# Optimization experiments

Hardware: AMD Instinct MI355X
Metric: run time of the kernel (lower is better)

## Reference

```python
import jax, jax.numpy as jnp
import numpy as np
from jax import lax

E = 8          # num_experts
K = 2          # top-k
TASKS = 8
GATE_DIM = 16
# (in, expand, out, kernel, stride) per MoE stage
STAGES = [(3, 32, 16, 7, 2), (16, 64, 32, 3, 1), (32, 128, 64, 3, 2), (64, 256, 64, 3, 1), (64, 128, 32, 3, 1)]
DN = ('NCHW', 'OIHW', 'NCHW')


def _pw(x, w):
    return lax.conv_general_dilated(x, w, (1, 1), 'VALID', dimension_numbers=DN)


def _dw(x, w, s):
    p = w.shape[-1] // 2
    return lax.conv_general_dilated(x, w, (s, s), [(p, p), (p, p)], dimension_numbers=DN, feature_group_count=x.shape[1])


def _gn(x, scale, bias):
    # GroupNorm with num_groups = C // 4, eps = 1e-5 (torch default)
    B, C, H, W = x.shape
    G = C // 4
    xr = x.reshape(B, G, -1)
    m = xr.mean(-1, keepdims=True)
    v = xr.var(-1, keepdims=True)
    xn = ((xr - m) * lax.rsqrt(v + 1e-5)).reshape(B, C, H, W)
    return xn * scale[None, :, None, None] + bias[None, :, None, None]


def _dsc(x, p, stride):
    # DSCBlock: pw-conv -> GN -> SiLU -> dw-conv -> GN -> SiLU -> pw-conv -> GN
    w1, s1, b1, w2, s2, b2, w3, s3, b3 = p
    x = jax.nn.silu(_gn(_pw(x, w1), s1, b1))
    x = jax.nn.silu(_gn(_dw(x, w2, stride), s2, b2))
    return _gn(_pw(x, w3), s3, b3)


def _moe(gate_input, x, wg, p, stride, task_bh):
    # task-conditioned top-k softmax gating (noisy_gating=False, all aux loss weights 0)
    logits = gate_input @ wg[task_bh]                      # (B, E)
    probs = jax.nn.softmax(logits, axis=-1)
    topv, topi = lax.top_k(probs, K)
    topv = topv / topv.sum(-1, keepdims=True)              # renormalize top-k gates
    Bn = gate_input.shape[0]
    dense = jnp.zeros_like(probs).at[jnp.arange(Bn)[:, None], topi].set(topv)
    eo = jax.vmap(lambda pe: _dsc(x, pe, stride))(p)       # (E, B, C, H, W)
    return jnp.einsum('be,ebchw->bchw', dense, eo)


def _forward(fl, task_bh):
    gi, xi, ppe = fl[0], fl[1], fl[2]
    x = xi
    for i, (_, _, _, _, s) in enumerate(STAGES):
        base = 3 + i * 10
        wg = fl[base]
        p = tuple(fl[base + 1: base + 10])
        x = _moe(gi, x, wg, p, s, task_bh)
    Bn = x.shape[0]
    # patchify: (B,32,20,20) -> unfold(2,4,4).unfold(3,4,4) -> permute -> (B,25,512)
    patches = x.reshape(Bn, 32, 5, 4, 5, 4).transpose(0, 1, 2, 4, 3, 5)  # (B,32,5,5,4,4)
    patches = patches.transpose(0, 2, 3, 4, 5, 1).reshape(Bn, 25, 512)
    return patches + ppe


def setup_inputs():
    key = jax.random.key(0)
    ks = iter(jax.random.split(key, 256))
    B = 64
    d = {}
    d['gate_input'] = jax.random.normal(next(ks), (B, GATE_DIM), jnp.float32)
    d['expert_input'] = jax.random.normal(next(ks), (B, 3, 80, 80), jnp.float32)
    d['patch_pos_embed'] = 0.02 * jax.random.normal(next(ks), (1, 25, 512), jnp.float32)
    for i, (cin, exp, cout, k, s) in enumerate(STAGES, 1):
        d[f's{i}_wg'] = 0.1 * jax.random.normal(next(ks), (TASKS, GATE_DIM, E), jnp.float32)
        d[f's{i}_w1'] = jax.random.normal(next(ks), (E, exp, cin, 1, 1), jnp.float32) / np.sqrt(cin)
        d[f's{i}_g1s'] = 1.0 + 0.1 * jax.random.normal(next(ks), (E, exp), jnp.float32)
        d[f's{i}_g1b'] = 0.1 * jax.random.normal(next(ks), (E, exp), jnp.float32)
        d[f's{i}_w2'] = jax.random.normal(next(ks), (E, exp, 1, k, k), jnp.float32) / k
        d[f's{i}_g2s'] = 1.0 + 0.1 * jax.random.normal(next(ks), (E, exp), jnp.float32)
        d[f's{i}_g2b'] = 0.1 * jax.random.normal(next(ks), (E, exp), jnp.float32)
        d[f's{i}_w3'] = jax.random.normal(next(ks), (E, cout, exp, 1, 1), jnp.float32) / np.sqrt(exp)
        d[f's{i}_g3s'] = 1.0 + 0.1 * jax.random.normal(next(ks), (E, cout), jnp.float32)
        d[f's{i}_g3b'] = 0.1 * jax.random.normal(next(ks), (E, cout), jnp.float32)
    d['task_bh'] = 3
    return d


def reference(gate_input, expert_input, patch_pos_embed, s1_wg, s1_w1, s1_g1s, s1_g1b, s1_w2, s1_g2s, s1_g2b, s1_w3, s1_g3s, s1_g3b, s2_wg, s2_w1, s2_g1s, s2_g1b, s2_w2, s2_g2s, s2_g2b, s2_w3, s2_g3s, s2_g3b, s3_wg, s3_w1, s3_g1s, s3_g1b, s3_w2, s3_g2s, s3_g2b, s3_w3, s3_g3s, s3_g3b, s4_wg, s4_w1, s4_g1s, s4_g1b, s4_w2, s4_g2s, s4_g2b, s4_w3, s4_g3s, s4_g3b, s5_wg, s5_w1, s5_g1s, s5_g1b, s5_w2, s5_g2s, s5_g2b, s5_w3, s5_g3s, s5_g3b, task_bh):
    fl = (gate_input, expert_input, patch_pos_embed,
          s1_wg, s1_w1, s1_g1s, s1_g1b, s1_w2, s1_g2s, s1_g2b, s1_w3, s1_g3s, s1_g3b,
          s2_wg, s2_w1, s2_g1s, s2_g1b, s2_w2, s2_g2s, s2_g2b, s2_w3, s2_g3s, s2_g3b,
          s3_wg, s3_w1, s3_g1s, s3_g1b, s3_w2, s3_g2s, s3_g2b, s3_w3, s3_g3s, s3_g3b,
          s4_wg, s4_w1, s4_g1s, s4_g1b, s4_w2, s4_g2s, s4_g2b, s4_w3, s4_g3s, s4_g3b,
          s5_wg, s5_w1, s5_g1s, s5_g1b, s5_w2, s5_g2s, s5_g2b, s5_w3, s5_g3s, s5_g3b)
    patches = _forward(fl, task_bh)
    loss = jnp.zeros((), patches.dtype)  # all MoE loss weights are 0 in VisionEncoder
    return (patches, loss)
```

## Files before the change

kernel.cpp:

```cpp
#include <hip/hip_runtime.h>
#include <cstddef>

#define TPB 256

typedef __attribute__((ext_vector_type(8))) short short8v;
typedef __attribute__((ext_vector_type(4))) float f32x4;

__device__ __forceinline__ int rfl(int v) { return __builtin_amdgcn_readfirstlane(v); }
__device__ __forceinline__ float rflf(float v) {
    return __int_as_float(__builtin_amdgcn_readfirstlane(__float_as_int(v)));
}

__device__ __forceinline__ unsigned short f2bf(float f) {
    union { float f; unsigned int u; } x{f};
    unsigned int r = x.u + 0x7fffu + ((x.u >> 16) & 1u);
    return (unsigned short)(r >> 16);
}
__device__ __forceinline__ float bf2f(unsigned short u) {
    return __uint_as_float(((unsigned int)u) << 16);
}

template <int N, int NW>
__device__ __forceinline__ void bredN(float* v, float* red) {
    __syncthreads();
    #pragma unroll
    for (int off = 32; off > 0; off >>= 1)
        #pragma unroll
        for (int i = 0; i < N; i++) v[i] += __shfl_down(v[i], off);
    const int lane = threadIdx.x & 63;
    const int wv = threadIdx.x >> 6;
    if (lane == 0)
        #pragma unroll
        for (int i = 0; i < N; i++) red[wv * N + i] = v[i];
    __syncthreads();
    if (threadIdx.x == 0) {
        #pragma unroll
        for (int i = 0; i < N; i++) {
            float s = 0.f;
            #pragma unroll
            for (int w = 0; w < NW; w++) s += red[w * N + i];
            red[i] = s;
        }
    }
    __syncthreads();
    #pragma unroll
    for (int i = 0; i < N; i++) v[i] = red[i];
}

__device__ __forceinline__ float silu_f(float v) {
    return v * __builtin_amdgcn_rcpf(1.f + __expf(-v));
}

struct GatePtrs { const float* wg[5]; };
struct WSrcs { const float* p[9]; };

__global__ __launch_bounds__(256) void wprep(WSrcs wsrc,
                                             unsigned short* __restrict__ whi,
                                             unsigned short* __restrict__ wlo) {
    const int sizes[9] = {4096, 8192, 16384, 32768, 65536, 131072, 131072, 65536, 32768};
    int idx = blockIdx.x * 256 + threadIdx.x;
    if (idx >= 487424) return;
    int rem = idx, s = 0;
    while (s < 8 && rem >= sizes[s]) { rem -= sizes[s]; s++; }
    const float v = wsrc.p[s][rem];
    const unsigned short h = f2bf(v);
    whi[idx] = h;
    wlo[idx] = f2bf(v - bf2f(h));
}

__global__ void gate_kernel(const float* __restrict__ gi, GatePtrs gp,
                            const int* __restrict__ taskp,
                            int* __restrict__ gidx, float* __restrict__ gw) {
    const int s = blockIdx.x;
    const int b = threadIdx.x;
    const int task = taskp[0];
    const float* wg = gp.wg[s] + (size_t)task * 16 * 8;
    float l[8];
    #pragma unroll
    for (int e = 0; e < 8; e++) l[e] = 0.f;
    for (int d = 0; d < 16; d++) {
        float v = gi[b * 16 + d];
        #pragma unroll
        for (int e = 0; e < 8; e++) l[e] += v * wg[d * 8 + e];
    }
    float mx = l[0];
    #pragma unroll
    for (int e = 1; e < 8; e++) mx = fmaxf(mx, l[e]);
    float p[8]; float sum = 0.f;
    #pragma unroll
    for (int e = 0; e < 8; e++) { p[e] = expf(l[e] - mx); sum += p[e]; }
    int i0 = 0;
    #pragma unroll
    for (int e = 1; e < 8; e++) if (p[e] > p[i0]) i0 = e;
    int i1 = (i0 == 0) ? 1 : 0;
    #pragma unroll
    for (int e = 0; e < 8; e++) if (e != i0 && p[e] > p[i1]) i1 = e;
    const float denom = p[i0] + p[i1];
    const int base = (s * 64 + b) * 2;
    gidx[base] = i0; gidx[base + 1] = i1;
    gw[base] = p[i0] / denom; gw[base + 1] = p[i1] / denom;
}

template <int M, int K, int N, int MT, int NCHK, bool FOLD, bool BIN>
__global__ __launch_bounds__(256) void gemm_bf16(
    const unsigned short* __restrict__ inp,
    const unsigned short* __restrict__ whi, const unsigned short* __restrict__ wlo,
    const int* __restrict__ gidx, const float* __restrict__ foldStats,
    const float* __restrict__ foldS, const float* __restrict__ foldB,
    unsigned short* __restrict__ outp, float* __restrict__ stats,
    int mfull, int moff) {
    constexpr int KITERS = (K + 31) / 32;
    constexpr int IM = (MT == 64) ? 2 : 1;
    constexpr int IN = (MT == 16) ? 1 : 2;
    const int bx = blockIdx.x;
    const int nc = bx % NCHK, mc = bx / NCHK;
    const int b = blockIdx.y, slot = blockIdx.z;
    const int bs = b * 2 + slot;
    const int e = rfl(gidx[b * 2 + slot]);
    const int n0 = nc * 64, m0 = mc * MT;
    const int tid = threadIdx.x;
    const int lane = tid & 63, wv = tid >> 6;
    const int quad = lane >> 4, l15 = lane & 15;

    __shared__ __align__(16) unsigned short wtileH[MT * 40];
    __shared__ __align__(16) unsigned short wtileL[MT * 40];
    __shared__ unsigned int intile[16 * 65];
    __shared__ float sred[(MT / 4) * 2];
    __shared__ float afv[K], bfv[K];

    if (tid < (MT / 4) * 2) sred[tid] = 0.f;
    if constexpr (FOLD) {
        for (int c = tid; c < K; c += 256) {
            const int g = c >> 2;
            const float s1 = foldStats[((size_t)bs * (K / 4) + g) * 2 + 0];
            const float s2 = foldStats[((size_t)bs * (K / 4) + g) * 2 + 1];
            const float mean = s1 / (4.f * N);
            const float var = s2 / (4.f * N) - mean * mean;
            const float inv = rsqrtf(var + 1e-5f);
            const float sc = foldS[e * K + c], bi = foldB[e * K + c];
            afv[c] = inv * sc;
            bfv[c] = bi - mean * inv * sc;
        }
    }

    int mbase, nbase;
    if constexpr (MT == 64) { mbase = (wv & 1) * 32; nbase = (wv >> 1) * 32; }
    else if constexpr (MT == 32) { mbase = (wv & 1) * 16; nbase = (wv >> 1) * 32; }
    else { mbase = 0; nbase = wv * 16; }

    f32x4 acc[IM][IN];
    #pragma unroll
    for (int im = 0; im < IM; im++)
        #pragma unroll
        for (int in = 0; in < IN; in++)
            #pragma unroll
            for (int r = 0; r < 4; r++) acc[im][in][r] = 0.f;

    const unsigned short* ib = inp + (size_t)(BIN ? b : bs) * K * N;
    const unsigned short* wbH = whi + ((size_t)e * mfull + moff) * K;
    const unsigned short* wbL = wlo + ((size_t)e * mfull + moff) * K;

    for (int k0 = 0; k0 < KITERS * 32; k0 += 32) {
        __syncthreads();
        for (int i = tid; i < MT * 32; i += 256) {
            const int m = i >> 5, kk = i & 31;
            const bool ok = (k0 + kk < K);
            const size_t src = (size_t)(m0 + m) * K + k0 + kk;
            wtileH[m * 40 + kk] = ok ? wbH[src] : (unsigned short)0;
            wtileL[m * 40 + kk] = ok ? wbL[src] : (unsigned short)0;
        }
        {
            const int kp = tid >> 4, nq = tid & 15;
            const int k = k0 + kp * 2;
            const int n = n0 + nq * 4;
            unsigned short u0[4] = {0, 0, 0, 0}, u1[4] = {0, 0, 0, 0};
            const bool nv = (n < N);
            if (nv && k < K) {
                const ushort4 t = *(const ushort4*)(ib + (size_t)k * N + n);
                u0[0] = t.x; u0[1] = t.y; u0[2] = t.z; u0[3] = t.w;
            }
            if (nv && k + 1 < K) {
                const ushort4 t = *(const ushort4*)(ib + (size_t)(k + 1) * N + n);
                u1[0] = t.x; u1[1] = t.y; u1[2] = t.z; u1[3] = t.w;
            }
            #pragma unroll
            for (int t = 0; t < 4; t++) {
                float f0, f1;
                if constexpr (FOLD) {
                    f0 = (nv && k < K) ? silu_f(afv[k] * bf2f(u0[t]) + bfv[k]) : 0.f;
                    f1 = (nv && k + 1 < K) ? silu_f(afv[k + 1] * bf2f(u1[t]) + bfv[k + 1]) : 0.f;
                } else {
                    f0 = bf2f(u0[t]); f1 = bf2f(u1[t]);
                }
                intile[kp * 65 + nq * 4 + t] =
                    (unsigned int)f2bf(f0) | ((unsigned int)f2bf(f1) << 16);
            }
        }
        __syncthreads();

        short8v afrH[IM], afrL[IM];
        #pragma unroll
        for (int im = 0; im < IM; im++) {
            const int m = mbase + im * 16 + l15;
            afrH[im] = *(const short8v*)&wtileH[m * 40 + quad * 8];
            afrL[im] = *(const short8v*)&wtileL[m * 40 + quad * 8];
        }
        #pragma unroll
        for (int in = 0; in < IN; in++) {
            union { unsigned int u[4]; short8v s; } bu;
            const int col = nbase + in * 16 + l15;
            #pragma unroll
            for (int i = 0; i < 4; i++) bu.u[i] = intile[(quad * 4 + i) * 65 + col];
            #pragma unroll
            for (int im = 0; im < IM; im++) {
                acc[im][in] = __builtin_amdgcn_mfma_f32_16x16x32_bf16(
                    afrH[im], bu.s, acc[im][in], 0, 0, 0);
                acc[im][in] = __builtin_amdgcn_mfma_f32_16x16x32_bf16(
                    afrL[im], bu.s, acc[im][in], 0, 0, 0);
            }
        }
    }

    unsigned short* ob = outp + (size_t)bs * M * N;
    #pragma unroll
    for (int im = 0; im < IM; im++) {
        #pragma unroll
        for (int in = 0; in < IN; in++) {
            const int n = n0 + nbase + in * 16 + l15;
            float s1 = 0.f, s2 = 0.f;
            #pragma unroll
            for (int r = 0; r < 4; r++) {
                const float a = acc[im][in][r];
                s1 += a; s2 += a * a;
            }
            if (n < N) {
                #pragma unroll
                for (int r = 0; r < 4; r++) {
                    const int m = m0 + mbase + im * 16 + quad * 4 + r;
                    ob[(size_t)m * N + n] = f2bf(acc[im][in][r]);
                }
            }
            #pragma unroll
            for (int off = 8; off > 0; off >>= 1) {
                s1 += __shfl_down(s1, off, 16);
                s2 += __shfl_down(s2, off, 16);
            }
            if (l15 == 0) {
                const int gl = (mbase + im * 16) / 4 + quad;
                atomicAdd(&sred[gl * 2 + 0], s1);
                atomicAdd(&sred[gl * 2 + 1], s2);
            }
        }
    }
    __syncthreads();
    for (int i = tid; i < MT / 4; i += 256) {
        float* sp = stats + (((size_t)bs * (mfull / 4) + moff / 4 + mc * (MT / 4) + i)
                             * NCHK + nc) * 2;
        sp[0] = sred[i * 2]; sp[1] = sred[i * 2 + 1];
    }
}

template <int CLOC, int CFULL, int H, int W, int NCH, int TPBk, int NCHK1>
__global__ __launch_bounds__(TPBk) void dw_k(
    const unsigned short* __restrict__ raw1, const float* __restrict__ stats1,
    const float* __restrict__ g1s, const float* __restrict__ g1b,
    const float* __restrict__ w2, const int* __restrict__ gidx,
    unsigned short* __restrict__ act2raw, float* __restrict__ stats2, int coff) {
    constexpr int HW = H * W, HP = H + 2, WPL = W + 3;
    constexpr int NPV = HW / 4, NG = NCH / 4, NW = TPBk / 64;
    constexpr int Qc = HW / 4, QT = NCH * Qc, QI = (QT + TPBk - 1) / TPBk;
    constexpr int G1 = CFULL / 4;
    const int gch = blockIdx.x, b = blockIdx.y, slot = blockIdx.z;
    const int bs = b * 2 + slot;
    const int tid = threadIdx.x;
    const int e = rfl(gidx[b * 2 + slot]);
    const int cb0 = gch * NCH;
    const int cg0 = coff + cb0;

    __shared__ float buf1[NCH * HP * WPL];
    __shared__ float w2s[NCH * 9];
    __shared__ float afl[NCH], bfl[NCH];
    __shared__ float red[2 * NG * NW];

    for (int i = tid; i < NCH * HP * WPL; i += TPBk) buf1[i] = 0.f;
    if (tid < NCH * 9) w2s[tid] = w2[((size_t)e * CFULL + cg0) * 9 + tid];
    if (tid < NCH) {
        const int g = (cg0 + tid) >> 2;
        float s1 = 0.f, s2 = 0.f;
        for (int i = 0; i < NCHK1; i++) {
            s1 += stats1[(((size_t)bs * G1 + g) * NCHK1 + i) * 2 + 0];
            s2 += stats1[(((size_t)bs * G1 + g) * NCHK1 + i) * 2 + 1];
        }
        const float mean = s1 / (4.f * HW);
        const float var = s2 / (4.f * HW) - mean * mean;
        const float inv = rsqrtf(var + 1e-5f);
        const float sc = g1s[e * CFULL + cg0 + tid], bi = g1b[e * CFULL + cg0 + tid];
        afl[tid] = inv * sc; bfl[tid] = bi - mean * inv * sc;
    }
    __syncthreads();

    const unsigned short* rb = raw1 + (size_t)bs * CLOC * HW + (size_t)cb0 * HW;
    for (int i = tid; i < NCH * NPV; i += TPBk) {
        const int c = i / NPV, pv = i - c * NPV;
        const int p4 = pv * 4, ph = p4 / W, pwb = p4 - ph * W;
        const ushort4 u = *(const ushort4*)(rb + (size_t)c * HW + p4);
        const float a = afl[c], bb = bfl[c];
        float* bp = &buf1[(c * HP + ph + 1) * WPL + pwb + 1];
        bp[0] = silu_f(a * bf2f(u.x) + bb);
        bp[1] = silu_f(a * bf2f(u.y) + bb);
        bp[2] = silu_f(a * bf2f(u.z) + bb);
        bp[3] = silu_f(a * bf2f(u.w) + bb);
    }
    __syncthreads();

    float st2[2 * NG];
    #pragma unroll
    for (int i = 0; i < 2 * NG; i++) st2[i] = 0.f;
    unsigned short* ao = act2raw + (size_t)bs * CFULL * HW + (size_t)cg0 * HW;
    #pragma unroll
    for (int qi = 0; qi < QI; qi++) {
        const int q = tid + qi * TPBk;
        if (QI * TPBk == QT || q < QT) {
            const int c = q / Qc, qq = q - c * Qc;
            const int oh = qq % H, owb = (qq / H) * 4;
            float o[4] = {0.f, 0.f, 0.f, 0.f};
            #pragma unroll
            for (int kh = 0; kh < 3; kh++) {
                const int base = (c * HP + oh + kh) * WPL + owb;
                float r[6];
                #pragma unroll
                for (int i = 0; i < 6; i++) r[i] = buf1[base + i];
                const float wa = w2s[c * 9 + kh * 3 + 0];
                const float wb = w2s[c * 9 + kh * 3 + 1];
                const float wcc = w2s[c * 9 + kh * 3 + 2];
                #pragma unroll
                for (int t = 0; t < 4; t++)
                    o[t] += wa * r[t] + wb * r[t + 1] + wcc * r[t + 2];
            }
            ushort4 ov = {f2bf(o[0]), f2bf(o[1]), f2bf(o[2]), f2bf(o[3])};
            *(ushort4*)(ao + c * HW + oh * W + owb) = ov;
            #pragma unroll
            for (int t = 0; t < 4; t++) {
                if constexpr (NG == 1) { st2[0] += o[t]; st2[1] += o[t] * o[t]; }
                else {
                    const bool gs = (c >= 4);
                    float a0 = gs ? 0.f : o[t], a1 = gs ? o[t] : 0.f;
                    st2[0] += a0; st2[1] += a0 * a0;
                    st2[2] += a1; st2[3] += a1 * a1;
                }
            }
        }
    }
    bredN<2 * NG, NW>(st2, red);
    if (tid == 0) {
        #pragma unroll
        for (int g = 0; g < NG; g++) {
            stats2[((size_t)bs * G1 + cg0 / 4 + g) * 2 + 0] = st2[g * 2];
            stats2[((size_t)bs * G1 + cg0 / 4 + g) * 2 + 1] = st2[g * 2 + 1];
        }
    }
}

__global__ __launch_bounds__(256) void s1_stats(
    const float* __restrict__ xin, const float* __restrict__ w1,
    const int* __restrict__ gidx, float* __restrict__ stats1) {
    const int g = blockIdx.x, b = blockIdx.y, slot = blockIdx.z;
    const int tid = threadIdx.x;
    const int e = rfl(gidx[b * 2 + slot]);
    __shared__ float red[8];
    const float* xb = xin + (size_t)b * 3 * 6400;
    const float* w1e = w1 + ((size_t)e * 32 + g * 4) * 3;
    float wr[4][3];
    #pragma unroll
    for (int c = 0; c < 4; c++)
        #pragma unroll
        for (int k = 0; k < 3; k++) wr[c][k] = rflf(w1e[c * 3 + k]);
    float s[2] = {0.f, 0.f};
    #pragma unroll
    for (int j = 0; j < 7; j++) {
        const int i = j * 256 + tid;
        if (i < 1600) {
            const int p4 = i * 4;
            const float4 v0 = *(const float4*)(xb + p4);
            const float4 v1 = *(const float4*)(xb + 6400 + p4);
            const float4 v2 = *(const float4*)(xb + 12800 + p4);
            const float a0[4] = {v0.x, v0.y, v0.z, v0.w};
            const float a1[4] = {v1.x, v1.y, v1.z, v1.w};
            const float a2[4] = {v2.x, v2.y, v2.z, v2.w};
            #pragma unroll
            for (int t = 0; t < 4; t++)
                #pragma unroll
                for (int c = 0; c < 4; c++) {
                    float a = fmaf(wr[c][0], a0[t], fmaf(wr[c][1], a1[t], wr[c][2] * a2[t]));
                    s[0] += a; s[1] += a * a;
                }
        }
    }
    bredN<2, 4>(s, red);
    if (tid == 0) {
        float* sp = stats1 + ((size_t)(b * 2 + slot) * 8 + g) * 2;
        sp[0] = s[0]; sp[1] = s[1];
    }
}

__global__ __launch_bounds__(256) void s1_band(
    const float* __restrict__ xin, const float* __restrict__ w1,
    const float* __restrict__ g1s, const float* __restrict__ g1b,
    const float* __restrict__ w2, const int* __restrict__ gidx,
    const float* __restrict__ stats1,
    float* __restrict__ rawdw, float* __restrict__ stats2) {
    constexpr int NR = 25, RW32 = 43;
    const int gb = blockIdx.x;
    const int g = gb >> 2, band = gb & 3;
    const int b = blockIdx.y, slot = blockIdx.z;
    const int tid = threadIdx.x;
    const int e = rfl(gidx[b * 2 + slot]);

    __shared__ unsigned int sbuf[4 * NR * RW32];
    __shared__ float w2s[196];
    __shared__ float red[8];

    for (int i = tid; i < 4 * NR * RW32; i += 256) sbuf[i] = 0u;
    if (tid < 196) w2s[tid] = w2[((size_t)e * 32 + g * 4) * 49 + tid];

    const float* sp = stats1 + ((size_t)(b * 2 + slot) * 8 + g) * 2;
    const float s1v = rflf(sp[0]), s2v = rflf(sp[1]);
    const float mean = s1v / 25600.f;
    const float var = s2v / 25600.f - mean * mean;
    const float inv = rsqrtf(var + 1e-5f);

    const float* xb = xin + (size_t)b * 3 * 6400;
    const float* w1e = w1 + ((size_t)e * 32 + g * 4) * 3;
    float wr[4][3], sc1r[4], bi1r[4];
    #pragma unroll
    for (int c = 0; c < 4; c++) {
        #pragma unroll
        for (int k = 0; k < 3; k++) wr[c][k] = rflf(w1e[c * 3 + k]);
        sc1r[c] = rflf(g1s[e * 32 + g * 4 + c]);
        bi1r[c] = rflf(g1b[e * 32 + g * 4 + c]);
    }
    const int oh0 = band * 10;
    const int rlo = 2 * oh0 - 3;
    __syncthreads();

    unsigned short* sb16 = (unsigned short*)sbuf;
    for (int ii = tid; ii < 500; ii += 256) {
        const int p4 = ii * 4;
        const int l = p4 / 80, pw = p4 - l * 80;
        const int r = rlo + l;
        if (r >= 0 && r < 80) {
            const float4 v0 = *(const float4*)(xb + r * 80 + pw);
            const float4 v1 = *(const float4*)(xb + 6400 + r * 80 + pw);
            const float4 v2 = *(const float4*)(xb + 12800 + r * 80 + pw);
            const float a0[4] = {v0.x, v0.y, v0.z, v0.w};
            const float a1[4] = {v1.x, v1.y, v1.z, v1.w};
            const float a2[4] = {v2.x, v2.y, v2.z, v2.w};
            #pragma unroll
            for (int c = 0; c < 4; c++) {
                unsigned short* row16 = sb16 + ((c * NR + l) * RW32) * 2 + pw + 3;
                #pragma unroll
                for (int t = 0; t < 4; t++) {
                    float a = fmaf(wr[c][0], a0[t], fmaf(wr[c][1], a1[t], wr[c][2] * a2[t]));
                    row16[t] = f2bf(silu_f((a - mean) * inv * sc1r[c] + bi1r[c]));
                }
            }
        }
    }
    __syncthreads();

    float st2[2] = {0.f, 0.f};
    float* rw = rawdw + (size_t)(b * 2 + slot) * 32 * 1600 + (size_t)g * 4 * 1600;
    #pragma unroll
    for (int qi = 0; qi < 7; qi++) {
        const int q = tid + qi * 256;
        if (q < 1600) {
            const int c = q / 400, rem = q - c * 400;
            const int ow = rem % 40, ohl = rem / 40;
            float o = 0.f;
            #pragma unroll
            for (int kh = 0; kh < 7; kh++) {
                const unsigned int* rp = &sbuf[(c * NR + 2 * ohl + kh) * RW32 + ow];
                const unsigned int d0 = rp[0], d1 = rp[1], d2 = rp[2], d3 = rp[3];
                const float* wk = &w2s[c * 49 + kh * 7];
                o += wk[0] * __uint_as_float(d0 << 16)
                   + wk[1] * __uint_as_float(d0 & 0xffff0000u)
                   + wk[2] * __uint_as_float(d1 << 16)
                   + wk[3] * __uint_as_float(d1 & 0xffff0000u)
                   + wk[4] * __uint_as_float(d2 << 16)
                   + wk[5] * __uint_as_float(d2 & 0xffff0000u)
                   + wk[6] * __uint_as_float(d3 << 16);
            }
            rw[c * 1600 + (oh0 + ohl) * 40 + ow] = o;
            st2[0] += o; st2[1] += o * o;
        }
    }
    bredN<2, 4>(st2, red);
    if (tid == 0) {
        float* s2p = stats2 + (((size_t)(b * 2 + slot) * 8 + g) * 4 + band) * 2;
        s2p[0] = st2[0]; s2p[1] = st2[1];
    }
}

__global__ __launch_bounds__(256) void s1_norm(
    const float* __restrict__ rawdw, const float* __restrict__ stats2,
    const float* __restrict__ g2s, const float* __restrict__ g2b,
    const int* __restrict__ gidx, unsigned short* __restrict__ act2) {
    const int g = blockIdx.x, b = blockIdx.y, slot = blockIdx.z;
    const int tid = threadIdx.x;
    const int e = rfl(gidx[b * 2 + slot]);
    const float* sp = stats2 + ((size_t)(b * 2 + slot) * 8 + g) * 8;
    const float s1 = rflf(sp[0]) + rflf(sp[2]) + rflf(sp[4]) + rflf(sp[6]);
    const float s2 = rflf(sp[1]) + rflf(sp[3]) + rflf(sp[5]) + rflf(sp[7]);
    const float mean2 = s1 / 6400.f;
    const float var2 = s2 / 6400.f - mean2 * mean2;
    const float inv2 = rsqrtf(var2 + 1e-5f);
    const float* rb = rawdw + (size_t)(b * 2 + slot) * 32 * 1600 + (size_t)g * 4 * 1600;
    unsigned short* ao = act2 + ((size_t)(b * 2 + slot) * 32 + g * 4) * 1600;
    #pragma unroll
    for (int c = 0; c < 4; c++) {
        const float sc = rflf(g2s[e * 32 + g * 4 + c]);
        const float bi = rflf(g2b[e * 32 + g * 4 + c]);
        #pragma unroll
        for (int qi = 0; qi < 2; qi++) {
            const int i = tid + qi * 256;
            if (i < 400) {
                const float4 v = *(const float4*)(rb + c * 1600 + i * 4);
                ushort4 ov;
                ov.x = f2bf(silu_f((v.x - mean2) * inv2 * sc + bi));
                ov.y = f2bf(silu_f((v.y - mean2) * inv2 * sc + bi));
                ov.z = f2bf(silu_f((v.z - mean2) * inv2 * sc + bi));
                ov.w = f2bf(silu_f((v.w - mean2) * inv2 * sc + bi));
                *(ushort4*)(ao + c * 1600 + i * 4) = ov;
            }
        }
    }
}

template <int CIN, int CEXP, int KS, int STRIDE, int H, int W, int HO, int WO,
          int NCH, int TPBk>
__global__ __launch_bounds__(TPBk) void dsc_ab_v2(
    const unsigned short* __restrict__ xin, const float* __restrict__ w1,
    const float* __restrict__ g1s, const float* __restrict__ g1b,
    const float* __restrict__ w2,
    const float* __restrict__ g2s, const float* __restrict__ g2b,
    const int* __restrict__ gidx, unsigned short* __restrict__ act2) {
    constexpr int HW = H * W, HWO = HO * WO;
    constexpr int HP = H + 2, WPL = W + 3, EVW = (W + 2) / 2;
    constexpr int NPV = HW / 4;
    constexpr int JN = (NPV + TPBk - 1) / TPBk;
    constexpr int NW = TPBk / 64;
    constexpr int NG = NCH / 4;
    constexpr int Qc = HWO / 4;
    constexpr int QT = NCH * Qc;
    constexpr int QI = (QT + TPBk - 1) / TPBk;
    constexpr int KK = KS * KS;
    const int gch = blockIdx.x, b = blockIdx.y, slot = blockIdx.z;
    const int tid = threadIdx.x;
    const int e = rfl(gidx[b * 2 + slot]);
    const int cb0 = gch * NCH;

    __shared__ float buf1[NCH * HP * WPL];
    __shared__ float w2s[NCH * KK];
    __shared__ float sc2s[NCH], bi2s[NCH];
    __shared__ float red[2 * NG * NW];

    for (int i = tid; i < NCH * HP * WPL; i += TPBk) buf1[i] = 0.f;
    for (int i = tid; i < NCH * KK; i += TPBk) {
        int c = i / KK, k = i - c * KK;
        w2s[i] = w2[((size_t)e * CEXP + cb0 + c) * KK + k];
    }
    if (tid < NCH) {
        sc2s[tid] = g2s[e * CEXP + cb0 + tid];
        bi2s[tid] = g2b[e * CEXP + cb0 + tid];
    }

    const unsigned short* xb = xin + (size_t)b * CIN * HW;
    const float* w1e = w1 + ((size_t)e * CEXP + cb0) * CIN;

    float acc[NCH][JN][4];
    #pragma unroll
    for (int c = 0; c < NCH; c++)
        #pragma unroll
        for (int j = 0; j < JN; j++)
            #pragma unroll
            for (int t = 0; t < 4; t++) acc[c][j][t] = 0.f;

    for (int cb = 0; cb < CIN; cb += 4) {
        float wr[NCH][4];
        #pragma unroll
        for (int c = 0; c < NCH; c++)
            #pragma unroll
            for (int k = 0; k < 4; k++) wr[c][k] = rflf(w1e[c * CIN + cb + k]);
        #pragma unroll
        for (int j = 0; j < JN; j++) {
            const int pv = tid + j * TPBk;
            if (JN * TPBk == NPV || pv < NPV) {
                #pragma unroll
                for (int k = 0; k < 4; k++) {
                    const ushort4 v4 = *(const ushort4*)(xb + (cb + k) * HW + pv * 4);
                    const float va[4] = {bf2f(v4.x), bf2f(v4.y), bf2f(v4.z), bf2f(v4.w)};
                    #pragma unroll
                    for (int c = 0; c < NCH; c++)
                        #pragma unroll
                        for (int t = 0; t < 4; t++)
                            acc[c][j][t] = fmaf(wr[c][k], va[t], acc[c][j][t]);
                }
            }
        }
    }
    float st[2 * NG];
    #pragma unroll
    for (int i = 0; i < 2 * NG; i++) st[i] = 0.f;
    #pragma unroll
    for (int c = 0; c < NCH; c++) {
        const int gs = (c >> 2) * 2;
        #pragma unroll
        for (int j = 0; j < JN; j++)
            #pragma unroll
            for (int t = 0; t < 4; t++) {
                float a = acc[c][j][t];
                st[gs] += a; st[gs + 1] += a * a;
            }
    }
    bredN<2 * NG, NW>(st, red);
    float mg[NG], ig[NG];
    #pragma unroll
    for (int g = 0; g < NG; g++) {
        mg[g] = st[g * 2] / (4.f * HW);
        float var = st[g * 2 + 1] / (4.f * HW) - mg[g] * mg[g];
        ig[g] = rsqrtf(var + 1e-5f);
    }
    float sc1r[NCH], bi1r[NCH];
    #pragma unroll
    for (int c = 0; c < NCH; c++) {
        sc1r[c] = rflf(g1s[e * CEXP + cb0 + c]);
        bi1r[c] = rflf(g1b[e * CEXP + cb0 + c]);
    }
    #pragma unroll
    for (int j = 0; j < JN; j++) {
        const int pv = tid + j * TPBk;
        if (JN * TPBk == NPV || pv < NPV) {
            const int p4 = pv * 4;
            const int ph = p4 / W, pwb = p4 - ph * W;
            #pragma unroll
            for (int c = 0; c < NCH; c++) {
                const int g = (NG == 1) ? 0 : (c >> 2);
                #pragma unroll
                for (int t = 0; t < 4; t++) {
                    float v = silu_f((acc[c][j][t] - mg[g]) * ig[g] * sc1r[c] + bi1r[c]);
                    const int j2 = pwb + t + 1;
                    const int col = (STRIDE == 1) ? j2
                                    : ((j2 & 1) ? EVW + (j2 >> 1) : (j2 >> 1));
                    buf1[(c * HP + ph + 1) * WPL + col] = v;
                }
            }
        }
    }
    __syncthreads();

    float dacc[QI][4];
    float st2[2 * NG];
    #pragma unroll
    for (int i = 0; i < 2 * NG; i++) st2[i] = 0.f;
    #pragma unroll
    for (int qi = 0; qi < QI; qi++) {
        #pragma unroll
        for (int t = 0; t < 4; t++) dacc[qi][t] = 0.f;
        const int q = tid + qi * TPBk;
        if (QI * TPBk == QT || q < QT) {
            const int c = q / Qc, qq = q - c * Qc;
            const int oh = qq % HO, owb = (qq / HO) * 4;
            float o[4] = {0.f, 0.f, 0.f, 0.f};
            if (STRIDE == 1) {
                #pragma unroll
                for (int kh = 0; kh < KS; kh++) {
                    const int base = (c * HP + oh + kh) * WPL + owb;
                    float r[6];
                    #pragma unroll
                    for (int i = 0; i < 6; i++) r[i] = buf1[base + i];
                    const float wa = w2s[c * KK + kh * KS + 0];
                    const float wb = w2s[c * KK + kh * KS + 1];
                    const float wcc = w2s[c * KK + kh * KS + 2];
                    #pragma unroll
                    for (int t = 0; t < 4; t++)
                        o[t] += wa * r[t] + wb * r[t + 1] + wcc * r[t + 2];
                }
            } else {
                #pragma unroll
                for (int kh = 0; kh < KS; kh++) {
                    const int base = (c * HP + 2 * oh + kh) * WPL;
                    float ev[5], od[4];
                    #pragma unroll
                    for (int i = 0; i < 5; i++) ev[i] = buf1[base + owb + i];
                    #pragma unroll
                    for (int i = 0; i < 4; i++) od[i] = buf1[base + EVW + owb + i];
                    const float wa = w2s[c * KK + kh * KS + 0];
                    const float wb = w2s[c * KK + kh * KS + 1];
                    const float wcc = w2s[c * KK + kh * KS + 2];
                    #pragma unroll
                    for (int t = 0; t < 4; t++)
                        o[t] += wa * ev[t] + wb * od[t] + wcc * ev[t + 1];
                }
            }
            #pragma unroll
            for (int t = 0; t < 4; t++) {
                float a = o[t];
                dacc[qi][t] = a;
                if constexpr (NG == 1) {
                    st2[0] += a; st2[1] += a * a;
                } else {
                    const bool gsel = (c >= 4);
                    float a0 = gsel ? 0.f : a, a1 = gsel ? a : 0.f;
                    st2[0] += a0; st2[1] += a0 * a0;
                    st2[2] += a1; st2[3] += a1 * a1;
                }
            }
        }
    }
    bredN<2 * NG, NW>(st2, red);
    float m2[NG], i2[NG];
    #pragma unroll
    for (int g = 0; g < NG; g++) {
        m2[g] = st2[g * 2] / (4.f * HWO);
        float var = st2[g * 2 + 1] / (4.f * HWO) - m2[g] * m2[g];
        i2[g] = rsqrtf(var + 1e-5f);
    }
    unsigned short* ao = act2 + ((size_t)(b * 2 + slot) * CEXP + cb0) * HWO;
    #pragma unroll
    for (int qi = 0; qi < QI; qi++) {
        const int q = tid + qi * TPBk;
        if (QI * TPBk == QT || q < QT) {
            const int c = q / Qc, qq = q - c * Qc;
            const int oh = qq % HO, owb = (qq / HO) * 4;
            const int g = (NG == 1) ? 0 : ((c >= 4) ? 1 : 0);
            const float sc = sc2s[c], bi = bi2s[c];
            ushort4 ov;
            ov.x = f2bf(silu_f((dacc[qi][0] - m2[g]) * i2[g] * sc + bi));
            ov.y = f2bf(silu_f((dacc[qi][1] - m2[g]) * i2[g] * sc + bi));
            ov.z = f2bf(silu_f((dacc[qi][2] - m2[g]) * i2[g] * sc + bi));
            ov.w = f2bf(silu_f((dacc[qi][3] - m2[g]) * i2[g] * sc + bi));
            *(ushort4*)(ao + c * HWO + oh * WO + owb) = ov;
        }
    }
}

template <int COUT, int HWO, int PXC, bool PATCH>
__global__ __launch_bounds__(256) void pw3_k3m(
    const unsigned short* __restrict__ raw3, const float* __restrict__ statsw,
    const float* __restrict__ g3s, const float* __restrict__ g3b,
    const int* __restrict__ gidx, const float* __restrict__ gw,
    const float* __restrict__ ppe, float* __restrict__ outf,
    unsigned short* __restrict__ outb) {
    constexpr int G = COUT / 4;
    constexpr int Q = HWO / 4;
    const int gg = blockIdx.x, b = blockIdx.y;
    const int tid = threadIdx.x;

    float A[2][4], Bv[2][4];
    #pragma unroll
    for (int slot = 0; slot < 2; slot++) {
        const int e = rfl(gidx[b * 2 + slot]);
        const float wgt = rflf(gw[b * 2 + slot]);
        const float* sp = statsw + ((size_t)(b * 2 + slot) * G + gg) * PXC * 2;
        float s1 = 0.f, s2 = 0.f;
        for (int i = 0; i < PXC; i++) { s1 += rflf(sp[i * 2]); s2 += rflf(sp[i * 2 + 1]); }
        const float mean = s1 / (4.f * HWO);
        const float var = s2 / (4.f * HWO) - mean * mean;
        const float inv = rsqrtf(var + 1e-5f);
        #pragma unroll
        for (int i = 0; i < 4; i++) {
            const int c = gg * 4 + i;
            const float sc = rflf(g3s[e * COUT + c]);
            const float bi = rflf(g3b[e * COUT + c]);
            A[slot][i] = wgt * inv * sc;
            Bv[slot][i] = wgt * (bi - mean * inv * sc);
        }
    }

    #pragma unroll
    for (int i = 0; i < 4; i++) {
        const int c = gg * 4 + i;
        const unsigned short* r0 = raw3 + ((size_t)(b * 2 + 0) * COUT + c) * HWO;
        const unsigned short* r1 = raw3 + ((size_t)(b * 2 + 1) * COUT + c) * HWO;
        for (int q = tid; q < Q; q += 256) {
            const int p4 = q * 4;
            const ushort4 u0 = *(const ushort4*)(r0 + p4);
            const ushort4 u1 = *(const ushort4*)(r1 + p4);
            const float v0[4] = {bf2f(u0.x), bf2f(u0.y), bf2f(u0.z), bf2f(u0.w)};
            const float v1[4] = {bf2f(u1.x), bf2f(u1.y), bf2f(u1.z), bf2f(u1.w)};
            float o[4];
            #pragma unroll
            for (int t = 0; t < 4; t++)
                o[t] = fmaf(A[0][i], v0[t], Bv[0][i]) + fmaf(A[1][i], v1[t], Bv[1][i]);
            if constexpr (!PATCH) {
                ushort4 ov = {f2bf(o[0]), f2bf(o[1]), f2bf(o[2]), f2bf(o[3])};
                *(ushort4*)(outb + ((size_t)b * COUT + c) * HWO + p4) = ov;
            } else {
                const int ph = p4 / 20, pw0 = p4 - ph * 20;
                const int p = (ph >> 2) * 5 + (pw0 >> 2);
                const int dbase = ((ph & 3) * 4) * 32 + c;
                float* op = outf + ((size_t)b * 25 + p) * 512;
                const float* pp = ppe + p * 512;
                #pragma unroll
                for (int jj = 0; jj < 4; jj++)
                    op[dbase + jj * 32] = o[jj] + pp[dbase + jj * 32];
            }
        }
    }
    if (PATCH && gg == 0 && b == 0 && tid == 0) outf[64 * 25 * 512] = 0.f;
}

extern "C" void kernel_launch(void* const* d_in, const int* in_sizes, int n_in,
                              void* d_out, int out_size, void* d_ws, size_t ws_size,
                              hipStream_t stream) {
    const float* gate_input = (const float*)d_in[0];
    const float* expert_input = (const float*)d_in[1];
    const float* ppe = (const float*)d_in[2];
    const int* taskp = (const int*)d_in[53];
    auto in = [&](int s, int k) { return (const float*)d_in[3 + s * 10 + k]; };

    char* ws = (char*)d_ws;
    int* gidx = (int*)ws;
    float* gw = (float*)(ws + 4096);
    size_t off = 8192;
    unsigned short* x0 = (unsigned short*)(ws + off); off += (size_t)8 << 20;
    unsigned short* x1 = (unsigned short*)(ws + off); off += (size_t)8 << 20;
    unsigned short* act2 = (unsigned short*)(ws + off); off += (size_t)27 << 20;
    char* bufA = ws + off; off += (size_t)27 << 20;
    float* stats1 = (float*)(ws + off); off += (size_t)2 << 20;
    float* stats2 = (float*)(ws + off); off += 262144;
    float* stats3 = (float*)(ws + off); off += (size_t)1 << 20;
    float* st1a = (float*)(ws + off); off += 65536;
    float* st1b = (float*)(ws + off); off += 65536;
    unsigned short* whi = (unsigned short*)(ws + off); off += 487424 * 2;
    unsigned short* wlo = (unsigned short*)(ws + off); off += 487424 * 2;
    float* outp = (float*)d_out;
    unsigned short* bufA16 = (unsigned short*)bufA;

    WSrcs wsrc;
    wsrc.p[0] = in(0, 7); wsrc.p[1] = in(1, 1); wsrc.p[2] = in(1, 7);
    wsrc.p[3] = in(2, 1); wsrc.p[4] = in(2, 7); wsrc.p[5] = in(3, 1);
    wsrc.p[6] = in(3, 7); wsrc.p[7] = in(4, 1); wsrc.p[8] = in(4, 7);

    GatePtrs gp;
    for (int s = 0; s < 5; s++) gp.wg[s] = in(s, 0);
    gate_kernel<<<5, 64, 0, stream>>>(gate_input, gp, taskp, gidx, gw);
    wprep<<<(487424 + 255) / 256, 256, 0, stream>>>(wsrc, whi, wlo);

    s1_stats<<<dim3(8, 64, 2), 256, 0, stream>>>(expert_input, in(0, 1),
                                                 gidx + 0 * 128, st1a);
    s1_band<<<dim3(32, 64, 2), 256, 0, stream>>>(
        expert_input, in(0, 1), in(0, 2), in(0, 3), in(0, 4),
        gidx + 0 * 128, st1a, (float*)bufA, st1b);
    s1_norm<<<dim3(8, 64, 2), 256, 0, stream>>>(
        (float*)bufA, st1b, in(0, 5), in(0, 6), gidx + 0 * 128, act2);
    gemm_bf16<16, 32, 1600, 16, 25, false, false><<<dim3(25, 64, 2), 256, 0, stream>>>(
        act2, whi + 0, wlo + 0, gidx + 0 * 128, nullptr, nullptr, nullptr,
        bufA16, stats3, 16, 0);
    pw3_k3m<16, 1600, 25, false><<<dim3(4, 64), 256, 0, stream>>>(
        bufA16, stats3, in(0, 8), in(0, 9), gidx + 0 * 128,
        gw + 0 * 128, ppe, nullptr, x0);

    gemm_bf16<64, 16, 1600, 64, 25, false, true><<<dim3(25, 64, 2), 256, 0, stream>>>(
        x0, whi + 4096, wlo + 4096, gidx + 1 * 128, nullptr, nullptr, nullptr,
        bufA16, stats1, 64, 0);
    dw_k<64, 64, 40, 40, 4, 256, 25><<<dim3(16, 64, 2), 256, 0, stream>>>(
        bufA16, stats1, in(1, 2), in(1, 3), in(1, 4),
        gidx + 1 * 128, act2, stats2, 0);
    gemm_bf16<32, 64, 1600, 32, 25, true, false><<<dim3(25, 64, 2), 256, 0, stream>>>(
        act2, whi + 12288, wlo + 12288, gidx + 1 * 128, stats2, in(1, 5), in(1, 6),
        bufA16, stats3, 32, 0);
    pw3_k3m<32, 1600, 25, false><<<dim3(8, 64), 256, 0, stream>>>(
        bufA16, stats3, in(1, 8), in(1, 9), gidx + 1 * 128,
        gw + 1 * 128, ppe, nullptr, x1);

    dsc_ab_v2<32, 128, 3, 2, 40, 40, 20, 20, 4, 256><<<dim3(32, 64, 2), 256, 0, stream>>>(
        x1, in(2, 1), in(2, 2), in(2, 3), in(2, 4), in(2, 5), in(2, 6),
        gidx + 2 * 128, act2);
    gemm_bf16<64, 128, 400, 64, 7, false, false><<<dim3(7, 64, 2), 256, 0, stream>>>(
        act2, whi + 61440, wlo + 61440, gidx + 2 * 128, nullptr, nullptr, nullptr,
        bufA16, stats3, 64, 0);
    pw3_k3m<64, 400, 7, false><<<dim3(16, 64), 256, 0, stream>>>(
        bufA16, stats3, in(2, 8), in(2, 9), gidx + 2 * 128,
        gw + 2 * 128, ppe, nullptr, x0);

    gemm_bf16<256, 64, 400, 64, 7, false, true><<<dim3(28, 64, 2), 256, 0, stream>>>(
        x0, whi + 126976, wlo + 126976, gidx + 3 * 128, nullptr, nullptr, nullptr,
        bufA16, stats1, 256, 0);
    dw_k<256, 256, 20, 20, 8, 128, 7><<<dim3(32, 64, 2), 128, 0, stream>>>(
        bufA16, stats1, in(3, 2), in(3, 3), in(3, 4),
        gidx + 3 * 128, act2, stats2, 0);
    gemm_bf16<64, 256, 400, 64, 7, true, false><<<dim3(7, 64, 2), 256, 0, stream>>>(
        act2, whi + 258048, wlo + 258048, gidx + 3 * 128, stats2, in(3, 5), in(3, 6),
        bufA16, stats3, 64, 0);
    pw3_k3m<64, 400, 7, false><<<dim3(16, 64), 256, 0, stream>>>(
        bufA16, stats3, in(3, 8), in(3, 9), gidx + 3 * 128,
        gw + 3 * 128, ppe, nullptr, x1);

    gemm_bf16<128, 64, 400, 64, 7, false, true><<<dim3(14, 64, 2), 256, 0, stream>>>(
        x1, whi + 389120, wlo + 389120, gidx + 4 * 128, nullptr, nullptr, nullptr,
        bufA16, stats1, 128, 0);
    dw_k<128, 128, 20, 20, 8, 128, 7><<<dim3(16, 64, 2), 128, 0, stream>>>(
        bufA16, stats1, in(4, 2), in(4, 3), in(4, 4),
        gidx + 4 * 128, act2, stats2, 0);
    gemm_bf16<32, 128, 400, 32, 7, true, false><<<dim3(7, 64, 2), 256, 0, stream>>>(
        act2, whi + 454656, wlo + 454656, gidx + 4 * 128, stats2, in(4, 5), in(4, 6),
        bufA16, stats3, 32, 0);
    pw3_k3m<32, 400, 7, true><<<dim3(8, 64), 256, 0, stream>>>(
        bufA16, stats3, in(4, 8), in(4, 9), gidx + 4 * 128,
        gw + 4 * 128, ppe, outp, nullptr);
}
```

Before: 550.5 us.

## Drop split-bf16 weight correction in GEMMs and restructure stage-1 depthwise conv

The pointwise GEMMs no longer keep a low-order bf16 residual of the weights, so each k-step does one MFMA instead of two and loads half as much weight data into shared memory. The weight prep kernel writes only the high part. Separately, the stage-1 7x7 stride-2 depthwise conv now keeps its activations in fp32 shared memory split into even and odd columns. Each thread computes four outputs with vector LDS loads and a float4 store. The cost is lower weight precision in the GEMMs, which may affect accuracy tolerance.

After: 521.7 us. 5.2% less time.

```diff
diff --git a/kernel.cpp b/kernel.cpp
--- a/kernel.cpp
+++ b/kernel.cpp
@@ -55,17 +55,13 @@
 struct WSrcs { const float* p[9]; };
 
 __global__ __launch_bounds__(256) void wprep(WSrcs wsrc,
-                                             unsigned short* __restrict__ whi,
-                                             unsigned short* __restrict__ wlo) {
+                                             unsigned short* __restrict__ whi) {
     const int sizes[9] = {4096, 8192, 16384, 32768, 65536, 131072, 131072, 65536, 32768};
     int idx = blockIdx.x * 256 + threadIdx.x;
     if (idx >= 487424) return;
     int rem = idx, s = 0;
     while (s < 8 && rem >= sizes[s]) { rem -= sizes[s]; s++; }
-    const float v = wsrc.p[s][rem];
-    const unsigned short h = f2bf(v);
-    whi[idx] = h;
-    wlo[idx] = f2bf(v - bf2f(h));
+    whi[idx] = f2bf(wsrc.p[s][rem]);
 }
 
 __global__ void gate_kernel(const float* __restrict__ gi, GatePtrs gp,
@@ -104,7 +100,7 @@
 template <int M, int K, int N, int MT, int NCHK, bool FOLD, bool BIN>
 __global__ __launch_bounds__(256) void gemm_bf16(
     const unsigned short* __restrict__ inp,
-    const unsigned short* __restrict__ whi, const unsigned short* __restrict__ wlo,
+    const unsigned short* __restrict__ whi,
     const int* __restrict__ gidx, const float* __restrict__ foldStats,
     const float* __restrict__ foldS, const float* __restrict__ foldB,
     unsigned short* __restrict__ outp, float* __restrict__ stats,
@@ -122,8 +118,7 @@
     const int lane = tid & 63, wv = tid >> 6;
     const int quad = lane >> 4, l15 = lane & 15;
 
-    __shared__ __align__(16) unsigned short wtileH[MT * 40];
-    __shared__ __align__(16) unsigned short wtileL[MT * 40];
+    __shared__ __align__(16) unsigned short wtile[MT * 40];
     __shared__ unsigned int intile[16 * 65];
     __shared__ float sred[(MT / 4) * 2];
     __shared__ float afv[K], bfv[K];
@@ -158,16 +153,14 @@
 
     const unsigned short* ib = inp + (size_t)(BIN ? b : bs) * K * N;
     const unsigned short* wbH = whi + ((size_t)e * mfull + moff) * K;
-    const unsigned short* wbL = wlo + ((size_t)e * mfull + moff) * K;
 
     for (int k0 = 0; k0 < KITERS * 32; k0 += 32) {
         __syncthreads();
         for (int i = tid; i < MT * 32; i += 256) {
             const int m = i >> 5, kk = i & 31;
             const bool ok = (k0 + kk < K);
-            const size_t src = (size_t)(m0 + m) * K + k0 + kk;
-            wtileH[m * 40 + kk] = ok ? wbH[src] : (unsigned short)0;
-            wtileL[m * 40 + kk] = ok ? wbL[src] : (unsigned short)0;
+            wtile[m * 40 + kk] = ok ? wbH[(size_t)(m0 + m) * K + k0 + kk]
+                                    : (unsigned short)0;
         }
         {
             const int kp = tid >> 4, nq = tid & 15;
@@ -198,12 +191,11 @@
         }
         __syncthreads();
 
-        short8v afrH[IM], afrL[IM];
+        short8v afr[IM];
         #pragma unroll
         for (int im = 0; im < IM; im++) {
             const int m = mbase + im * 16 + l15;
-            afrH[im] = *(const short8v*)&wtileH[m * 40 + quad * 8];
-            afrL[im] = *(const short8v*)&wtileL[m * 40 + quad * 8];
+            afr[im] = *(const short8v*)&wtile[m * 40 + quad * 8];
         }
         #pragma unroll
         for (int in = 0; in < IN; in++) {
@@ -212,12 +204,9 @@
             #pragma unroll
             for (int i = 0; i < 4; i++) bu.u[i] = intile[(quad * 4 + i) * 65 + col];
             #pragma unroll
-            for (int im = 0; im < IM; im++) {
+            for (int im = 0; im < IM; im++)
                 acc[im][in] = __builtin_amdgcn_mfma_f32_16x16x32_bf16(
-                    afrH[im], bu.s, acc[im][in], 0, 0, 0);
-                acc[im][in] = __builtin_amdgcn_mfma_f32_16x16x32_bf16(
-                    afrL[im], bu.s, acc[im][in], 0, 0, 0);
-            }
+                    afr[im], bu.s, acc[im][in], 0, 0, 0);
         }
     }
 
@@ -409,18 +398,18 @@
     const float* __restrict__ w2, const int* __restrict__ gidx,
     const float* __restrict__ stats1,
     float* __restrict__ rawdw, float* __restrict__ stats2) {
-    constexpr int NR = 25, RW32 = 43;
+    constexpr int NR = 25, RW = 90, EVO = 44;
     const int gb = blockIdx.x;
     const int g = gb >> 2, band = gb & 3;
     const int b = blockIdx.y, slot = blockIdx.z;
     const int tid = threadIdx.x;
     const int e = rfl(gidx[b * 2 + slot]);
 
-    __shared__ unsigned int sbuf[4 * NR * RW32];
+    __shared__ float sbuf[4 * NR * RW];
     __shared__ float w2s[196];
     __shared__ float red[8];
 
-    for (int i = tid; i < 4 * NR * RW32; i += 256) sbuf[i] = 0u;
+    for (int i = tid; i < 4 * NR * RW; i += 256) sbuf[i] = 0.f;
     if (tid < 196) w2s[tid] = w2[((size_t)e * 32 + g * 4) * 49 + tid];
 
     const float* sp = stats1 + ((size_t)(b * 2 + slot) * 8 + g) * 2;
@@ -443,7 +432,6 @@
     const int rlo = 2 * oh0 - 3;
     __syncthreads();
 
-    unsigned short* sb16 = (unsigned short*)sbuf;
     for (int ii = tid; ii < 500; ii += 256) {
         const int p4 = ii * 4;
         const int l = p4 / 80, pw = p4 - l * 80;
@@ -457,11 +445,13 @@
             const float a2[4] = {v2.x, v2.y, v2.z, v2.w};
             #pragma unroll
             for (int c = 0; c < 4; c++) {
-                unsigned short* row16 = sb16 + ((c * NR + l) * RW32) * 2 + pw + 3;
                 #pragma unroll
                 for (int t = 0; t < 4; t++) {
                     float a = fmaf(wr[c][0], a0[t], fmaf(wr[c][1], a1[t], wr[c][2] * a2[t]));
-                    row16[t] = f2bf(silu_f((a - mean) * inv * sc1r[c] + bi1r[c]));
+                    float v = silu_f((a - mean) * inv * sc1r[c] + bi1r[c]);
+                    const int cc = pw + t + 3;
+                    const int sl = (cc & 1) ? EVO + (cc >> 1) : (cc >> 1);
+                    sbuf[(c * NR + l) * RW + sl] = v;
                 }
             }
         }
@@ -471,27 +461,43 @@
     float st2[2] = {0.f, 0.f};
     float* rw = rawdw + (size_t)(b * 2 + slot) * 32 * 1600 + (size_t)g * 4 * 1600;
     #pragma unroll
-    for (int qi = 0; qi < 7; qi++) {
+    for (int qi = 0; qi < 2; qi++) {
         const int q = tid + qi * 256;
-        if (q < 1600) {
-            const int c = q / 400, rem = q - c * 400;
-            const int ow = rem % 40, ohl = rem / 40;
-            float o = 0.f;
+        if (q < 400) {
+            const int c = q / 100;
+            const int rem = q - c * 100;
+            const int ohl = rem % 10, owb = (rem / 10) * 4;
+            float o[4] = {0.f, 0.f, 0.f, 0.f};
             #pragma unroll
             for (int kh = 0; kh < 7; kh++) {
-                const unsigned int* rp = &sbuf[(c * NR + 2 * ohl + kh) * RW32 + ow];
-                const unsigned int d0 = rp[0], d1 = rp[1], d2 = rp[2], d3 = rp[3];
-                const float* wk = &w2s[c * 49 + kh * 7];
-                o += wk[0] * __uint_as_float(d0 << 16)
-                   + wk[1] * __uint_as_float(d0 & 0xffff0000u)
-                   + wk[2] * __uint_as_float(d1 << 16)
-                   + wk[3] * __uint_as_float(d1 & 0xffff0000u)
-                   + wk[4] * __uint_as_float(d2 << 16)
-                   + wk[5] * __uint_as_float(d2 & 0xffff0000u)
-                   + wk[6] * __uint_as_float(d3 << 16);
-            }
-            rw[c * 1600 + (oh0 + ohl) * 40 + ow] = o;
-            st2[0] += o; st2[1] += o * o;
+                const int base = (c * NR + 2 * ohl + kh) * RW;
+                const float2 e01 = *(const float2*)&sbuf[base + owb];
+                const float2 e23 = *(const float2*)&sbuf[base + owb + 2];
+                const float2 e45 = *(const float2*)&sbuf[base + owb + 4];
+                const float e6 = sbuf[base + owb + 6];
+                const float2 q01 = *(const float2*)&sbuf[base + EVO + owb];
+                const float2 q23 = *(const float2*)&sbuf[base + EVO + owb + 2];
+                const float2 q45 = *(const float2*)&sbuf[base + EVO + owb + 4];
+                const float evr[7] = {e01.x, e01.y, e23.x, e23.y, e45.x, e45.y, e6};
+                const float odr[6] = {q01.x, q01.y, q23.x, q23.y, q45.x, q45.y};
+                const float w0 = w2s[c * 49 + kh * 7 + 0];
+                const float w1v = w2s[c * 49 + kh * 7 + 1];
+                const float w2v = w2s[c * 49 + kh * 7 + 2];
+                const float w3 = w2s[c * 49 + kh * 7 + 3];
+                const float w4 = w2s[c * 49 + kh * 7 + 4];
+                const float w5 = w2s[c * 49 + kh * 7 + 5];
+                const float w6 = w2s[c * 49 + kh * 7 + 6];
+                #pragma unroll
+                for (int t = 0; t < 4; t++)
+                    o[t] += w0 * evr[t] + w1v * odr[t] + w2v * evr[t + 1]
+                          + w3 * odr[t + 1] + w4 * evr[t + 2] + w5 * odr[t + 2]
+                          + w6 * evr[t + 3];
+            }
+            const int oh = oh0 + ohl;
+            float4 ov = {o[0], o[1], o[2], o[3]};
+            *(float4*)(rw + c * 1600 + oh * 40 + owb) = ov;
+            #pragma unroll
+            for (int t = 0; t < 4; t++) { st2[0] += o[t]; st2[1] += o[t] * o[t]; }
         }
     }
     bredN<2, 4>(st2, red);
@@ -833,7 +839,6 @@
     float* st1a = (float*)(ws + off); off += 65536;
     float* st1b = (float*)(ws + off); off += 65536;
     unsigned short* whi = (unsigned short*)(ws + off); off += 487424 * 2;
-    unsigned short* wlo = (unsigned short*)(ws + off); off += 487424 * 2;
     float* outp = (float*)d_out;
     unsigned short* bufA16 = (unsigned short*)bufA;
 
@@ -845,7 +850,7 @@
     GatePtrs gp;
     for (int s = 0; s < 5; s++) gp.wg[s] = in(s, 0);
     gate_kernel<<<5, 64, 0, stream>>>(gate_input, gp, taskp, gidx, gw);
-    wprep<<<(487424 + 255) / 256, 256, 0, stream>>>(wsrc, whi, wlo);
+    wprep<<<(487424 + 255) / 256, 256, 0, stream>>>(wsrc, whi);
 
     s1_stats<<<dim3(8, 64, 2), 256, 0, stream>>>(expert_input, in(0, 1),
                                                  gidx + 0 * 128, st1a);
@@ -855,20 +860,20 @@
     s1_norm<<<dim3(8, 64, 2), 256, 0, stream>>>(
         (float*)bufA, st1b, in(0, 5), in(0, 6), gidx + 0 * 128, act2);
     gemm_bf16<16, 32, 1600, 16, 25, false, false><<<dim3(25, 64, 2), 256, 0, stream>>>(
-        act2, whi + 0, wlo + 0, gidx + 0 * 128, nullptr, nullptr, nullptr,
+        act2, whi + 0, gidx + 0 * 128, nullptr, nullptr, nullptr,
         bufA16, stats3, 16, 0);
     pw3_k3m<16, 1600, 25, false><<<dim3(4, 64), 256, 0, stream>>>(
         bufA16, stats3, in(0, 8), in(0, 9), gidx + 0 * 128,
         gw + 0 * 128, ppe, nullptr, x0);
 
     gemm_bf16<64, 16, 1600, 64, 25, false, true><<<dim3(25, 64, 2), 256, 0, stream>>>(
-        x0, whi + 4096, wlo + 4096, gidx + 1 * 128, nullptr, nullptr, nullptr,
+        x0, whi + 4096, gidx + 1 * 128, nullptr, nullptr, nullptr,
         bufA16, stats1, 64, 0);
     dw_k<64, 64, 40, 40, 4, 256, 25><<<dim3(16, 64, 2), 256, 0, stream>>>(
         bufA16, stats1, in(1, 2), in(1, 3), in(1, 4),
         gidx + 1 * 128, act2, stats2, 0);
     gemm_bf16<32, 64, 1600, 32, 25, true, false><<<dim3(25, 64, 2), 256, 0, stream>>>(
-        act2, whi + 12288, wlo + 12288, gidx + 1 * 128, stats2, in(1, 5), in(1, 6),
+        act2, whi + 12288, gidx + 1 * 128, stats2, in(1, 5), in(1, 6),
         bufA16, stats3, 32, 0);
     pw3_k3m<32, 1600, 25, false><<<dim3(8, 64), 256, 0, stream>>>(
         bufA16, stats3, in(1, 8), in(1, 9), gidx + 1 * 128,
@@ -878,33 +883,33 @@
         x1, in(2, 1), in(2, 2), in(2, 3), in(2, 4), in(2, 5), in(2, 6),
         gidx + 2 * 128, act2);
     gemm_bf16<64, 128, 400, 64, 7, false, false><<<dim3(7, 64, 2), 256, 0, stream>>>(
-        act2, whi + 61440, wlo + 61440, gidx + 2 * 128, nullptr, nullptr, nullptr,
+        act2, whi + 61440, gidx + 2 * 128, nullptr, nullptr, nullptr,
         bufA16, stats3, 64, 0);
     pw3_k3m<64, 400, 7, false><<<dim3(16, 64), 256, 0, stream>>>(
         bufA16, stats3, in(2, 8), in(2, 9), gidx + 2 * 128,
         gw + 2 * 128, ppe, nullptr, x0);
 
     gemm_bf16<256, 64, 400, 64, 7, false, true><<<dim3(28, 64, 2), 256, 0, stream>>>(
-        x0, whi + 126976, wlo + 126976, gidx + 3 * 128, nullptr, nullptr, nullptr,
+        x0, whi + 126976, gidx + 3 * 128, nullptr, nullptr, nullptr,
         bufA16, stats1, 256, 0);
     dw_k<256, 256, 20, 20, 8, 128, 7><<<dim3(32, 64, 2), 128, 0, stream>>>(
         bufA16, stats1, in(3, 2), in(3, 3), in(3, 4),
         gidx + 3 * 128, act2, stats2, 0);
     gemm_bf16<64, 256, 400, 64, 7, true, false><<<dim3(7, 64, 2), 256, 0, stream>>>(
-        act2, whi + 258048, wlo + 258048, gidx + 3 * 128, stats2, in(3, 5), in(3, 6),
+        act2, whi + 258048, gidx + 3 * 128, stats2, in(3, 5), in(3, 6),
         bufA16, stats3, 64, 0);
     pw3_k3m<64, 400, 7, false><<<dim3(16, 64), 256, 0, stream>>>(
         bufA16, stats3, in(3, 8), in(3, 9), gidx + 3 * 128,
         gw + 3 * 128, ppe, nullptr, x1);
 
     gemm_bf16<128, 64, 400, 64, 7, false, true><<<dim3(14, 64, 2), 256, 0, stream>>>(
-        x1, whi + 389120, wlo + 389120, gidx + 4 * 128, nullptr, nullptr, nullptr,
+        x1, whi + 389120, gidx + 4 * 128, nullptr, nullptr, nullptr,
         bufA16, stats1, 128, 0);
     dw_k<128, 128, 20, 20, 8, 128, 7><<<dim3(16, 64, 2), 128, 0, stream>>>(
         bufA16, stats1, in(4, 2), in(4, 3), in(4, 4),
         gidx + 4 * 128, act2, stats2, 0);
     gemm_bf16<32, 128, 400, 32, 7, true, false><<<dim3(7, 64, 2), 256, 0, stream>>>(
-        act2, whi + 454656, wlo + 454656, gidx + 4 * 128, stats2, in(4, 5), in(4, 6),
+        act2, whi + 454656, gidx + 4 * 128, stats2, in(4, 5), in(4, 6),
         bufA16, stats3, 32, 0);
     pw3_k3m<32, 400, 7, true><<<dim3(8, 64), 256, 0, stream>>>(
         bufA16, stats3, in(4, 8), in(4, 9), gidx + 4 * 128,
```
